# Optimization experiments

Measured on AMD Instinct MI355X. Metric: run time of the kernel, lower is better.

The kernel has to match this reference:

```python
import jax, jax.numpy as jnp
import numpy as np

PASSES = 5
NUM_EDGE_SETS = 3
B, N, D = 8, 20000, 128
E = 64000
HID, OUT = 80, 10


def setup_inputs() -> dict:
    key = jax.random.key(0)
    ks = jax.random.split(key, 8)
    nodes = jax.random.normal(ks[0], (B, N, D), dtype=jnp.float32)
    problem_type = jax.random.normal(ks[1], (B, 1), dtype=jnp.float32)
    # edges[b, k, e] = (dst, src); index_add target is column 0, gathered source is column 1
    edges = jax.random.randint(ks[2], (B, NUM_EDGE_SETS, E, 2), 0, N, dtype=jnp.int32)
    w1 = jax.random.normal(ks[3], (D + 1, HID), jnp.float32) / np.sqrt(D + 1).astype(np.float32)
    b1 = jnp.zeros((HID,), jnp.float32)
    w2 = jax.random.normal(ks[4], (HID, HID), jnp.float32) / np.sqrt(HID).astype(np.float32)
    b2 = jnp.zeros((HID,), jnp.float32)
    w3 = jax.random.normal(ks[5], (HID, OUT), jnp.float32) / np.sqrt(HID).astype(np.float32)
    b3 = jnp.zeros((OUT,), jnp.float32)
    return {"nodes": nodes, "problem_type": problem_type, "w1": w1, "b1": b1,
            "w2": w2, "b2": b2, "w3": w3, "b3": b3, "edges": edges}


def _message_pass(nodes_g, edges_g):
    # nodes_g: [N, D]; edges_g: [K, E, 2] with (dst, src)
    inc = jnp.zeros_like(nodes_g)
    for k in range(NUM_EDGE_SETS):  # small fixed set of edge types
        dst = edges_g[k, :, 0]
        src = edges_g[k, :, 1]
        inc = inc + jax.ops.segment_sum(nodes_g[src], dst, num_segments=N)
    return nodes_g + inc


def _forward(nodes, problem_type, w1, b1, w2, b2, w3, b3, edges):
    step = jax.vmap(_message_pass)  # over batch of graphs

    def body(n, _):
        return step(n, edges), None

    nodes, _ = jax.lax.scan(body, nodes, None, length=PASSES)
    pooled = nodes.sum(axis=1)                       # [B, D]
    y = jnp.log(pooled)
    y = jnp.where(jnp.isnan(y), 0.0, y)              # nan -> 0
    y = jax.nn.relu(y)
    finite_max = jnp.max(jnp.where(jnp.isinf(y), -jnp.inf, y), axis=1, keepdims=True)
    y = jnp.where(y == jnp.inf, finite_max, y)       # +inf -> max finite entry
    x = jnp.concatenate([y, problem_type], axis=1)   # [B, D+1]
    x = jax.nn.leaky_relu(x @ w1 + b1)
    x = jax.nn.leaky_relu(x @ w2 + b2)
    return x @ w3 + b3                               # [B, OUT]


def reference(nodes, problem_type, w1, b1, w2, b2, w3, b3, edges):
    return _forward(nodes, problem_type, w1, b1, w2, b2, w3, b3, edges)
```

## Files before the change

### kernel.cpp

```cpp
#include <hip/hip_runtime.h>
#include <cmath>

#define NB 8
#define NN 20000
#define ND 128
#define NE_TOT 192000

#define GSZ 640
#define NG 32
#define ECHUNK 8000
#define NCHUNK 24
#define CSUB 384
#define FIX (NCHUNK * CSUB)
#define KPT (FIX / 1024)
#define JMAX 40

#define PBS 256
#define NPB ((NN + PBS - 1) / PBS)

__device__ float          g_w0[NB * NN];
__device__ float          g_w1[NB * NN];
__device__ int            g_ccnt[NB][NCHUNK][NG];
__device__ unsigned int   g_bucket[(size_t)NB * NG * FIX];
__device__ int            g_deg[NB * NN];
__device__ unsigned short g_pT[(size_t)NB * JMAX * NN];
__device__ float          g_ppart[NB * NPB * ND];

__global__ void distK(const int* __restrict__ edges) {
    __shared__ int cur[NG];
    const int b = blockIdx.x / NCHUNK, c = blockIdx.x % NCHUNK;
    const int t = threadIdx.x;
    if (t < NG) cur[t] = 0;
    __syncthreads();
    const int2* __restrict__ ep =
        (const int2*)edges + (size_t)b * NE_TOT + (size_t)c * ECHUNK;
    for (int i = t; i < ECHUNK; i += 256) {
        const int2 e = ep[i];
        const int g = (unsigned)e.y / GSZ;
        const int pos = atomicAdd(&cur[g], 1);
        if (pos < CSUB)
            g_bucket[((size_t)(b * NG + g)) * FIX + c * CSUB + pos] =
                (unsigned)e.x | ((unsigned)(e.y - g * GSZ) << 16);
    }
    __syncthreads();
    if (t < NG) g_ccnt[b][c][t] = min(cur[t], CSUB);
}

__global__ void __launch_bounds__(1024)
slotK() {
    __shared__ int hist[GSZ];
    __shared__ int cur[GSZ];
    __shared__ int ccnt[NCHUNK];
    const int b = blockIdx.y, g = blockIdx.x;
    const int t = threadIdx.x;

    const unsigned* __restrict__ bk = g_bucket + (size_t)(b * NG + g) * FIX + t;
    unsigned e[KPT];
#pragma unroll
    for (int k = 0; k < KPT; ++k) e[k] = bk[k * 1024];

    if (t < GSZ) { hist[t] = 0; cur[t] = 0; }
    if (t < NCHUNK) ccnt[t] = g_ccnt[b][t][g];
    __syncthreads();

    bool val[KPT];
#pragma unroll
    for (int k = 0; k < KPT; ++k) {
        const int p = k * 1024 + t;
        const int c = p / CSUB;
        val[k] = (p - c * CSUB) < ccnt[c];
        if (val[k]) atomicAdd(&hist[e[k] >> 16], 1);
    }
    __syncthreads();

    if (t < GSZ) {
        const int node = g * GSZ + t;
        if (node < NN) {
            const int d = hist[t];
            g_deg[b * NN + node] = min(d, JMAX);
            g_w1[b * NN + node]  = 1.0f + (float)d;
        }
    }
    __syncthreads();

    const size_t colbase = (size_t)b * JMAX * NN + g * GSZ;
#pragma unroll
    for (int k = 0; k < KPT; ++k)
        if (val[k]) {
            const int y = e[k] >> 16;
            const int j = atomicAdd(&cur[y], 1);
            if (j < JMAX)
                g_pT[colbase + (size_t)j * NN + y] = (unsigned short)(e[k] & 0xFFFF);
        }
}

template<int SRC>
__global__ void __launch_bounds__(256)
passT() {
    const int b = blockIdx.y;
    const int n = blockIdx.x * PBS + threadIdx.x;
    if (n >= NN) return;
    const float* __restrict__ wp = (SRC ? g_w1 : g_w0) + b * NN;
    float* __restrict__ wn       = (SRC ? g_w0 : g_w1) + b * NN;
    const int deg = g_deg[b * NN + n];
    const unsigned short* __restrict__ pT = g_pT + (size_t)b * JMAX * NN + n;
    float sum = wp[n];
#pragma unroll
    for (int j = 0; j < JMAX; ++j)
        if (j < deg) sum += wp[pT[(size_t)j * NN]];
    wn[n] = sum;
}

__global__ void __launch_bounds__(256)
pass5poolK(const float* __restrict__ nodes) {
    __shared__ float w5s[PBS];
    __shared__ __align__(16) float4 red[256];
    const int b = blockIdx.y, p = blockIdx.x;
    const int t = threadIdx.x;
    const int n0 = p * PBS;
    const int n  = n0 + t;
    const float* __restrict__ wp = g_w0 + b * NN;

    float w5 = 0.0f;
    if (n < NN) {
        const int deg = g_deg[b * NN + n];
        const unsigned short* __restrict__ pT = g_pT + (size_t)b * JMAX * NN + n;
        float sum = wp[n];
#pragma unroll
        for (int j = 0; j < JMAX; ++j)
            if (j < deg) sum += wp[pT[(size_t)j * NN]];
        w5 = sum;
    }
    w5s[t] = w5;
    __syncthreads();

    const int dslot = t & 31, rg = t >> 5;
    const int nrows = min(PBS, NN - n0);
    const float4* __restrict__ base = (const float4*)(nodes + (size_t)b * NN * ND);
    float4 aA = {0.f, 0.f, 0.f, 0.f}, aB = {0.f, 0.f, 0.f, 0.f};
    int row = rg;
    for (; row + 8 < nrows; row += 16) {
        const float wA = w5s[row], wB = w5s[row + 8];
        const float4 vA = base[(size_t)(n0 + row) * 32 + dslot];
        const float4 vB = base[(size_t)(n0 + row + 8) * 32 + dslot];
        aA.x += wA * vA.x; aA.y += wA * vA.y; aA.z += wA * vA.z; aA.w += wA * vA.w;
        aB.x += wB * vB.x; aB.y += wB * vB.y; aB.z += wB * vB.z; aB.w += wB * vB.w;
    }
    if (row < nrows) {
        const float wA = w5s[row];
        const float4 vA = base[(size_t)(n0 + row) * 32 + dslot];
        aA.x += wA * vA.x; aA.y += wA * vA.y; aA.z += wA * vA.z; aA.w += wA * vA.w;
    }
    float4 s4;
    s4.x = aA.x + aB.x; s4.y = aA.y + aB.y; s4.z = aA.z + aB.z; s4.w = aA.w + aB.w;
    red[t] = s4;
    __syncthreads();
    if (t < 32) {
        float4 s = red[t];
        for (int q = 1; q < 8; ++q) {
            const float4 o = red[q * 32 + t];
            s.x += o.x; s.y += o.y; s.z += o.z; s.w += o.w;
        }
        ((float4*)g_ppart)[((size_t)b * NPB + p) * 32 + t] = s;
    }
}

__global__ void reduceHeadK(const float* __restrict__ ptype,
                            const float* __restrict__ w1, const float* __restrict__ b1,
                            const float* __restrict__ w2, const float* __restrict__ b2,
                            const float* __restrict__ w3, const float* __restrict__ b3,
                            float* __restrict__ out) {
    __shared__ float sx[NB][ND + 1];
    __shared__ float h1s[NB][80];
    __shared__ float h2s[NB][80];
    const int t = threadIdx.x;
    const int b = t >> 7, d = t & 127;

    float s = 0.0f;
    for (int j = 0; j < NPB; ++j)
        s += g_ppart[((size_t)b * NPB + j) * ND + d];

    float y = logf(s);
    if (isnan(y)) y = 0.0f;
    y = fmaxf(y, 0.0f);
    sx[b][d] = y;
    __syncthreads();

    if (t < NB) {
        float fm = -INFINITY;
        for (int dd = 0; dd < ND; ++dd) {
            const float v = sx[t][dd];
            if (!isinf(v)) fm = fmaxf(fm, v);
        }
        for (int dd = 0; dd < ND; ++dd)
            if (isinf(sx[t][dd])) sx[t][dd] = fm;
        sx[t][ND] = ptype[t];
    }
    __syncthreads();

    if (t < NB * 80) {
        const int bb = t / 80, j = t - bb * 80;
        float v = b1[j];
        for (int k = 0; k < ND + 1; ++k) v += sx[bb][k] * w1[k * 80 + j];
        h1s[bb][j] = v > 0.0f ? v : 0.01f * v;
    }
    __syncthreads();

    if (t < NB * 80) {
        const int bb = t / 80, j = t - bb * 80;
        float v = b2[j];
        for (int k = 0; k < 80; ++k) v += h1s[bb][k] * w2[k * 80 + j];
        h2s[bb][j] = v > 0.0f ? v : 0.01f * v;
    }
    __syncthreads();

    if (t < NB * 10) {
        const int bb = t / 10, j = t - bb * 10;
        float v = b3[j];
        for (int k = 0; k < 80; ++k) v += h2s[bb][k] * w3[k * 10 + j];
        out[bb * 10 + j] = v;
    }
}

extern "C" void kernel_launch(void* const* d_in, const int* in_sizes, int n_in,
                              void* d_out, int out_size, void* d_ws, size_t ws_size,
                              hipStream_t stream) {
    const float* nodes = (const float*)d_in[0];
    const float* ptype = (const float*)d_in[1];
    const float* w1    = (const float*)d_in[2];
    const float* b1    = (const float*)d_in[3];
    const float* w2    = (const float*)d_in[4];
    const float* b2    = (const float*)d_in[5];
    const float* w3    = (const float*)d_in[6];
    const float* b3    = (const float*)d_in[7];
    const int*   edges = (const int*)d_in[8];
    float* out = (float*)d_out;

    distK<<<NB * NCHUNK, 256, 0, stream>>>(edges);
    slotK<<<dim3(NG, NB), 1024, 0, stream>>>();

    passT<1><<<dim3(NPB, NB), PBS, 0, stream>>>();
    passT<0><<<dim3(NPB, NB), PBS, 0, stream>>>();
    passT<1><<<dim3(NPB, NB), PBS, 0, stream>>>();

    pass5poolK<<<dim3(NPB, NB), PBS, 0, stream>>>(nodes);
    reduceHeadK<<<1, 1024, 0, stream>>>(ptype, w1, b1, w2, b2, w3, b3, out);
}
```

Baseline: 114.9 us.

## Split per-node gather across 4 thread groups, fuse head into pool via last-block

The middle message-passing kernels now use 512 threads per 128 nodes. Four thread groups each gather a strided quarter of the neighbour list, and the partial sums are combined in shared memory. This raises memory-level parallelism for the dependent index-then-value loads. Degrees are stored as 16-bit values to cut traffic. The separate head kernel is folded into the pooling kernel using an atomic completion counter, so the last block runs the reduction and MLP and one launch is saved. The cost is a serial tail inside the last block plus extra fences and atomics.

```diff
diff --git a/kernel.cpp b/kernel.cpp
--- a/kernel.cpp
+++ b/kernel.cpp
@@ -15,6 +15,7 @@
 #define KPT (FIX / 1024)
 #define JMAX 40
 
+#define PNB 157
 #define PBS 256
 #define NPB ((NN + PBS - 1) / PBS)
 
@@ -22,14 +23,16 @@
 __device__ float          g_w1[NB * NN];
 __device__ int            g_ccnt[NB][NCHUNK][NG];
 __device__ unsigned int   g_bucket[(size_t)NB * NG * FIX];
-__device__ int            g_deg[NB * NN];
+__device__ unsigned short g_degU[NB * NN];
 __device__ unsigned short g_pT[(size_t)NB * JMAX * NN];
 __device__ float          g_ppart[NB * NPB * ND];
+__device__ int            g_done;
 
 __global__ void distK(const int* __restrict__ edges) {
     __shared__ int cur[NG];
     const int b = blockIdx.x / NCHUNK, c = blockIdx.x % NCHUNK;
     const int t = threadIdx.x;
+    if (blockIdx.x == 0 && t == 0) g_done = 0;
     if (t < NG) cur[t] = 0;
     __syncthreads();
     const int2* __restrict__ ep =
@@ -77,8 +80,8 @@
         const int node = g * GSZ + t;
         if (node < NN) {
             const int d = hist[t];
-            g_deg[b * NN + node] = min(d, JMAX);
-            g_w1[b * NN + node]  = 1.0f + (float)d;
+            g_degU[b * NN + node] = (unsigned short)min(d, JMAX);
+            g_w1[b * NN + node]   = 1.0f + (float)d;
         }
     }
     __syncthreads();
@@ -95,26 +98,41 @@
 }
 
 template<int SRC>
-__global__ void __launch_bounds__(256)
-passT() {
-    const int b = blockIdx.y;
-    const int n = blockIdx.x * PBS + threadIdx.x;
-    if (n >= NN) return;
+__global__ void __launch_bounds__(512)
+passHO() {
+    __shared__ float sh[512];
+    const int b  = blockIdx.y;
+    const int nl = threadIdx.x & 127;
+    const int jg = threadIdx.x >> 7;
+    const int n  = blockIdx.x * 128 + nl;
     const float* __restrict__ wp = (SRC ? g_w1 : g_w0) + b * NN;
     float* __restrict__ wn       = (SRC ? g_w0 : g_w1) + b * NN;
-    const int deg = g_deg[b * NN + n];
-    const unsigned short* __restrict__ pT = g_pT + (size_t)b * JMAX * NN + n;
-    float sum = wp[n];
-#pragma unroll
-    for (int j = 0; j < JMAX; ++j)
-        if (j < deg) sum += wp[pT[(size_t)j * NN]];
-    wn[n] = sum;
+
+    float partial = 0.0f;
+    if (n < NN) {
+        const int deg = g_degU[b * NN + n];
+        const unsigned short* __restrict__ pT = g_pT + (size_t)b * JMAX * NN + n;
+#pragma unroll
+        for (int jj = 0; jj < 10; ++jj) {
+            const int j = jg + 4 * jj;
+            if (j < deg) partial += wp[pT[(size_t)j * NN]];
+        }
+    }
+    sh[threadIdx.x] = partial;
+    __syncthreads();
+    if (jg == 0 && n < NN)
+        wn[n] = wp[n] + ((sh[nl] + sh[128 + nl]) + (sh[256 + nl] + sh[384 + nl]));
 }
 
 __global__ void __launch_bounds__(256)
-pass5poolK(const float* __restrict__ nodes) {
+pass5poolHeadK(const float* __restrict__ nodes, const float* __restrict__ ptype,
+               const float* __restrict__ w1, const float* __restrict__ b1,
+               const float* __restrict__ w2, const float* __restrict__ b2,
+               const float* __restrict__ w3, const float* __restrict__ b3,
+               float* __restrict__ out) {
     __shared__ float w5s[PBS];
     __shared__ __align__(16) float4 red[256];
+    __shared__ int isLast;
     const int b = blockIdx.y, p = blockIdx.x;
     const int t = threadIdx.x;
     const int n0 = p * PBS;
@@ -123,7 +141,7 @@
 
     float w5 = 0.0f;
     if (n < NN) {
-        const int deg = g_deg[b * NN + n];
+        const int deg = g_degU[b * NN + n];
         const unsigned short* __restrict__ pT = g_pT + (size_t)b * JMAX * NN + n;
         float sum = wp[n];
 #pragma unroll
@@ -163,27 +181,31 @@
         }
         ((float4*)g_ppart)[((size_t)b * NPB + p) * 32 + t] = s;
     }
-}
-
-__global__ void reduceHeadK(const float* __restrict__ ptype,
-                            const float* __restrict__ w1, const float* __restrict__ b1,
-                            const float* __restrict__ w2, const float* __restrict__ b2,
-                            const float* __restrict__ w3, const float* __restrict__ b3,
-                            float* __restrict__ out) {
+
+    __syncthreads();
+    __threadfence();
+    if (t == 0) {
+        const int c = atomicAdd(&g_done, 1);
+        isLast = (c == NB * NPB - 1);
+    }
+    __syncthreads();
+    if (!isLast) return;
+    __threadfence();
+
     __shared__ float sx[NB][ND + 1];
     __shared__ float h1s[NB][80];
     __shared__ float h2s[NB][80];
-    const int t = threadIdx.x;
-    const int b = t >> 7, d = t & 127;
-
-    float s = 0.0f;
-    for (int j = 0; j < NPB; ++j)
-        s += g_ppart[((size_t)b * NPB + j) * ND + d];
-
-    float y = logf(s);
-    if (isnan(y)) y = 0.0f;
-    y = fmaxf(y, 0.0f);
-    sx[b][d] = y;
+
+    for (int i = t; i < NB * ND; i += 256) {
+        const int bb = i >> 7, d = i & 127;
+        float s = 0.0f;
+        for (int j = 0; j < NPB; ++j)
+            s += g_ppart[((size_t)bb * NPB + j) * ND + d];
+        float y = logf(s);
+        if (isnan(y)) y = 0.0f;
+        y = fmaxf(y, 0.0f);
+        sx[bb][d] = y;
+    }
     __syncthreads();
 
     if (t < NB) {
@@ -198,24 +220,24 @@
     }
     __syncthreads();
 
-    if (t < NB * 80) {
-        const int bb = t / 80, j = t - bb * 80;
+    for (int i = t; i < NB * 80; i += 256) {
+        const int bb = i / 80, j = i - bb * 80;
         float v = b1[j];
         for (int k = 0; k < ND + 1; ++k) v += sx[bb][k] * w1[k * 80 + j];
         h1s[bb][j] = v > 0.0f ? v : 0.01f * v;
     }
     __syncthreads();
 
-    if (t < NB * 80) {
-        const int bb = t / 80, j = t - bb * 80;
+    for (int i = t; i < NB * 80; i += 256) {
+        const int bb = i / 80, j = i - bb * 80;
         float v = b2[j];
         for (int k = 0; k < 80; ++k) v += h1s[bb][k] * w2[k * 80 + j];
         h2s[bb][j] = v > 0.0f ? v : 0.01f * v;
     }
     __syncthreads();
 
-    if (t < NB * 10) {
-        const int bb = t / 10, j = t - bb * 10;
+    for (int i = t; i < NB * 10; i += 256) {
+        const int bb = i / 10, j = i - bb * 10;
         float v = b3[j];
         for (int k = 0; k < 80; ++k) v += h2s[bb][k] * w3[k * 10 + j];
         out[bb * 10 + j] = v;
@@ -239,10 +261,10 @@
     distK<<<NB * NCHUNK, 256, 0, stream>>>(edges);
     slotK<<<dim3(NG, NB), 1024, 0, stream>>>();
 
-    passT<1><<<dim3(NPB, NB), PBS, 0, stream>>>();
-    passT<0><<<dim3(NPB, NB), PBS, 0, stream>>>();
-    passT<1><<<dim3(NPB, NB), PBS, 0, stream>>>();
-
-    pass5poolK<<<dim3(NPB, NB), PBS, 0, stream>>>(nodes);
-    reduceHeadK<<<1, 1024, 0, stream>>>(ptype, w1, b1, w2, b2, w3, b3, out);
-}
+    passHO<1><<<dim3(PNB, NB), 512, 0, stream>>>();
+    passHO<0><<<dim3(PNB, NB), 512, 0, stream>>>();
+    passHO<1><<<dim3(PNB, NB), 512, 0, stream>>>();
+
+    pass5poolHeadK<<<dim3(NPB, NB), PBS, 0, stream>>>(nodes, ptype,
+                                                      w1, b1, w2, b2, w3, b3, out);
+}
```

Measured after the change: 204.9 us (median of 2 runs). 78.4% more time.
